# Performance work log

Hardware: AMD Instinct MI355X
Metric: run time of the kernel (lower is better)

## Reference

```python
import jax, jax.numpy as jnp
import numpy as np

N = 131072      # points (rays x samples chunk)
E = 8           # spatial sub-networks (centroids)
DIN = 90        # encoded pos+dir features fed to sub-NeRFs (xyz_real=True -> x[:, 3:])
H = 256         # sub-NeRF hidden width
DOUT = 4        # rgb + sigma
MARGIN = 2.0    # boundary_margin
EPS = 1e-8


def setup_inputs() -> dict:
    key = jax.random.key(0)
    k = jax.random.split(key, 5)
    x_xyz = jax.random.uniform(k[0], (N, 3), dtype=jnp.float32)          # routing coords in [0,1)^3
    x_feat = jax.random.normal(k[1], (N, DIN), dtype=jnp.float32)        # encoded features
    x = jnp.concatenate([x_xyz, x_feat], axis=1)                         # [N, 3+DIN]
    centroids = jax.random.uniform(k[2], (E, 3), dtype=jnp.float32)
    W1 = jax.random.normal(k[3], (E, DIN, H), dtype=jnp.float32) * 0.05
    b1 = jnp.zeros((E, H), dtype=jnp.float32)
    W2 = jax.random.normal(k[4], (E, H, DOUT), dtype=jnp.float32) * 0.05
    b2 = jnp.zeros((E, DOUT), dtype=jnp.float32)
    return {"x": x, "centroids": centroids, "W1": W1, "b1": b1, "W2": W2, "b2": b2}


def reference(x, centroids, W1, b1, W2, b2):
    # --- centroid routing (torch.cdist equivalent) ---
    xyz = x[:, :3]                                                       # [N,3]
    d2 = jnp.sum((xyz[:, None, :] - centroids[None, :, :]) ** 2, axis=-1)
    dist = jnp.sqrt(jnp.maximum(d2, 0.0))                                # [N,E]
    inv = 1.0 / (dist + EPS)
    min_d = jnp.min(dist, axis=1, keepdims=True)                         # [N,1]
    inv = jnp.where(dist > MARGIN * min_d, 0.0, inv)                     # zero far experts
    weights = inv / jnp.sum(inv, axis=-1, keepdims=True)                 # [N,E], rows sum to 1

    # --- per-expert sub-NeRF MLP, weighted combine ---
    # Dense-equivalent of masked gather + weighted scatter-add: experts whose
    # weight is exactly 0 contribute nothing, matching the torch masked path.
    feat = x[:, 3:]                                                      # xyz_real=True -> drop xyz
    h = jax.nn.relu(jnp.einsum('nd,edh->enh', feat, W1) + b1[:, None, :])  # [E,N,H]
    out_e = jnp.einsum('enh,eho->eno', h, W2) + b2[:, None, :]             # [E,N,DOUT]
    return jnp.einsum('eno,ne->no', out_e, weights)                        # [N,DOUT]
```

## Files before the change

kernel.cpp:

```cpp
#include <hip/hip_runtime.h>

#define NPTS 131072
#define NE 8
#define DIN 90
#define NH 256

typedef __attribute__((ext_vector_type(8))) short bf16x8;
typedef __attribute__((ext_vector_type(4))) float f32x4;
typedef __attribute__((ext_vector_type(2))) float f32x2;
typedef __attribute__((ext_vector_type(4))) unsigned int u32x4;
typedef __attribute__((ext_vector_type(2))) unsigned int u32x2;
typedef __attribute__((ext_vector_type(4), aligned(4))) float f32x4a;
typedef __attribute__((ext_vector_type(2), aligned(4))) float f32x2a;

__device__ __forceinline__ unsigned short f2bf(float f) {
  unsigned int u = __float_as_uint(f);
  u += 0x7fffu + ((u >> 16) & 1u);
  return (unsigned short)(u >> 16);
}

__device__ __forceinline__ unsigned int pkbf(float f0, float f1) {
  unsigned int u0 = __float_as_uint(f0) + 0x7fffu;
  unsigned int u1 = __float_as_uint(f1) + 0x7fffu;
  return __builtin_amdgcn_perm(u1, u0, 0x07060302u);
}

__device__ __forceinline__ bf16x8 cvt8(f32x4 a, f32x4 b) {
  u32x4 r;
  r[0] = pkbf(a[0], a[1]);
  r[1] = pkbf(a[2], a[3]);
  r[2] = pkbf(b[0], b[1]);
  r[3] = pkbf(b[2], b[3]);
  return __builtin_bit_cast(bf16x8, r);
}

#define PREP_T (184320 + 12288 + 8192 + 24576)
__global__ __launch_bounds__(256) void prep(const float* __restrict__ W1,
                                            const float* __restrict__ W2,
                                            unsigned short* __restrict__ W1T,
                                            unsigned short* __restrict__ W2T) {
  int tid = blockIdx.x * 256 + threadIdx.x;
  if (tid < 184320) {
    float v = W1[tid];
    int n = tid & 255, r = tid >> 8;
    int kp = r % 90, e = r / 90;
    W1T[(size_t)(e * NH + n) * 96 + kp] = f2bf(v);
    return;
  }
  tid -= 184320;
  if (tid < 12288) {
    int kp = 90 + tid % 6, q = tid / 6;
    int n = q & 255, e = q >> 8;
    W1T[(size_t)(e * NH + n) * 96 + kp] = 0;
    return;
  }
  tid -= 12288;
  if (tid < 8192) {
    float v = W2[tid];
    int o = tid & 3, k = (tid >> 2) & 255, e = tid >> 10;
    W2T[(size_t)(e * 16 + o) * NH + k] = f2bf(v);
    return;
  }
  tid -= 8192;
  if (tid < 24576) {
    int k = tid & 255, q = tid >> 8;
    int o = 4 + q % 12, e = q / 12;
    W2T[(size_t)(e * 16 + o) * NH + k] = 0;
  }
}

__global__ __launch_bounds__(256, 3) void meganerf_main(
    const float* __restrict__ x, const float* __restrict__ cent,
    const float* __restrict__ b1, const float* __restrict__ b2,
    const unsigned short* __restrict__ W1T, const unsigned short* __restrict__ W2T,
    float* __restrict__ out) {
  __shared__ unsigned short sH[4 * 4096];
  __shared__ float sW[NE][64];
  __shared__ float sB2[64][4];

  const int t    = threadIdx.x;
  const int lane = t & 63;
  const int wid  = t >> 6;
  const int l15  = lane & 15;
  const int l4   = lane >> 4;
  const int row0 = blockIdx.x * 64;
  const int gbase = wid * 4096;

  bf16x8 bfr[4][3];
#pragma unroll
  for (int nf = 0; nf < 4; ++nf) {
    const float* gr = x + (size_t)(row0 + 16 * nf + l15) * 93 + 3;
    f32x4 v0, v1;
    v0 = *(const f32x4a*)(gr + 8 * l4);
    v1 = *(const f32x4a*)(gr + 8 * l4 + 4);
    bfr[nf][0] = cvt8(v0, v1);
    v0 = *(const f32x4a*)(gr + 32 + 8 * l4);
    v1 = *(const f32x4a*)(gr + 36 + 8 * l4);
    bfr[nf][1] = cvt8(v0, v1);
    if (l4 < 3) {
      v0 = *(const f32x4a*)(gr + 64 + 8 * l4);
      v1 = *(const f32x4a*)(gr + 68 + 8 * l4);
    } else {
      f32x2 tl = *(const f32x2a*)(gr + 88);
      v0[0] = tl[0]; v0[1] = tl[1]; v0[2] = 0.f; v0[3] = 0.f;
      v1[0] = 0.f; v1[1] = 0.f; v1[2] = 0.f; v1[3] = 0.f;
    }
    bfr[nf][2] = cvt8(v0, v1);
  }

  if (t < 64) {
    const float* gx = x + (size_t)(row0 + t) * 93;
    float px = gx[0], py = gx[1], pz = gx[2];
    float dist[NE], inv[NE];
    float mind = 3.4e38f;
#pragma unroll
    for (int e = 0; e < NE; ++e) {
      float dx = px - cent[e * 3 + 0];
      float dy = py - cent[e * 3 + 1];
      float dz = pz - cent[e * 3 + 2];
      float d2 = dx * dx + dy * dy + dz * dz;
      float d = sqrtf(fmaxf(d2, 0.f));
      dist[e] = d;
      inv[e] = 1.f / (d + 1e-8f);
      mind = fminf(mind, d);
    }
    float s = 0.f;
#pragma unroll
    for (int e = 0; e < NE; ++e) {
      if (dist[e] > 2.0f * mind) inv[e] = 0.f;
      s += inv[e];
    }
    float rs = 1.f / s;
    float bb[4] = {0.f, 0.f, 0.f, 0.f};
#pragma unroll
    for (int e = 0; e < NE; ++e) {
      float w = inv[e] * rs;
      sW[e][t] = w;
#pragma unroll
      for (int o = 0; o < 4; ++o) bb[o] += w * b2[e * 4 + o];
    }
#pragma unroll
    for (int o = 0; o < 4; ++o) sB2[t][o] = bb[o];
  }
  __syncthreads();

  f32x4 facc[4] = {{0.f, 0.f, 0.f, 0.f}, {0.f, 0.f, 0.f, 0.f},
                   {0.f, 0.f, 0.f, 0.f}, {0.f, 0.f, 0.f, 0.f}};

  for (int e = 0; e < NE; ++e) {
    bf16x8 bw[2];
#pragma unroll
    for (int ks2 = 0; ks2 < 2; ++ks2)
      bw[ks2] = *(const bf16x8*)(W2T + (size_t)(e * 16 + l15) * NH +
                                 128 * ks2 + 32 * wid + 8 * l4);
    float wv[4];
#pragma unroll
    for (int nf = 0; nf < 4; ++nf) wv[nf] = sW[e][16 * nf + l15];

#pragma unroll
    for (int c = 0; c < 2; ++c) {
      const int colbase = 128 * c + 32 * wid;
      bf16x8 w1f[2][3];
#pragma unroll
      for (int ks = 0; ks < 3; ++ks)
#pragma unroll
        for (int mf = 0; mf < 2; ++mf)
          w1f[mf][ks] = *(const bf16x8*)(W1T +
              (size_t)(e * NH + colbase + 16 * mf + l15) * 96 + 32 * ks + 8 * l4);
      f32x4 b1v[2];
#pragma unroll
      for (int mf = 0; mf < 2; ++mf)
        b1v[mf] = *(const f32x4*)(b1 + e * NH + colbase + 16 * mf + 4 * l4);
      f32x4 acc[2][4];
#pragma unroll
      for (int mf = 0; mf < 2; ++mf)
#pragma unroll
        for (int nf = 0; nf < 4; ++nf) acc[mf][nf] = b1v[mf];
#pragma unroll
      for (int ks = 0; ks < 3; ++ks)
#pragma unroll
        for (int mf = 0; mf < 2; ++mf)
#pragma unroll
          for (int nf = 0; nf < 4; ++nf)
            acc[mf][nf] = __builtin_amdgcn_mfma_f32_16x16x32_bf16(
                w1f[mf][ks], bfr[nf][ks], acc[mf][nf], 0, 0, 0);

#pragma unroll
      for (int mf = 0; mf < 2; ++mf) {
#pragma unroll
        for (int nf = 0; nf < 4; ++nf) {
          const float w = wv[nf];
          f32x4 a = acc[mf][nf];
          f32x2 p0, p1;
          p0[0] = a[0]; p0[1] = a[1];
          p1[0] = a[2]; p1[1] = a[3];
          const f32x2 z = {0.f, 0.f};
          p0 = __builtin_elementwise_max(p0, z) * w;
          p1 = __builtin_elementwise_max(p1, z) * w;
          u32x2 pk;
          pk[0] = pkbf(p0[0], p0[1]);
          pk[1] = pkbf(p1[0], p1[1]);
          *(u32x2*)&sH[gbase + ((nf * 2 + c) * 64 + (l15 + 16 * (2 * mf + (l4 >> 1)))) * 8 +
                       4 * (l4 & 1)] = pk;
        }
      }
    }

#pragma unroll
    for (int ks2 = 0; ks2 < 2; ++ks2)
#pragma unroll
      for (int rf = 0; rf < 4; ++rf) {
        bf16x8 ah = *(const bf16x8*)&sH[gbase + ((rf * 2 + ks2) * 64 + lane) * 8];
        facc[rf] = __builtin_amdgcn_mfma_f32_16x16x32_bf16(ah, bw[ks2], facc[rf], 0, 0, 0);
      }
  }

  __syncthreads();
  float* sOutP = (float*)sH;
  if (l15 < 4) {
#pragma unroll
    for (int rf = 0; rf < 4; ++rf)
#pragma unroll
      for (int r = 0; r < 4; ++r)
        sOutP[(wid * 64 + 16 * rf + 4 * l4 + r) * 4 + l15] = facc[rf][r];
  }
  __syncthreads();
  {
    const int row = t >> 2, o = t & 3;
    float v = sB2[row][o] + sOutP[(0 * 64 + row) * 4 + o] + sOutP[(1 * 64 + row) * 4 + o] +
              sOutP[(2 * 64 + row) * 4 + o] + sOutP[(3 * 64 + row) * 4 + o];
    out[row0 * 4 + t] = v;
  }
}

extern "C" void kernel_launch(void* const* d_in, const int* in_sizes, int n_in,
                              void* d_out, int out_size, void* d_ws, size_t ws_size,
                              hipStream_t stream) {
  const float* x    = (const float*)d_in[0];
  const float* cent = (const float*)d_in[1];
  const float* W1   = (const float*)d_in[2];
  const float* b1   = (const float*)d_in[3];
  const float* W2   = (const float*)d_in[4];
  const float* b2   = (const float*)d_in[5];
  float* out = (float*)d_out;

  unsigned short* W1T = (unsigned short*)d_ws;
  unsigned short* W2T = W1T + NE * NH * 96;

  prep<<<(PREP_T + 255) / 256, 256, 0, stream>>>(W1, W2, W1T, W2T);
  meganerf_main<<<NPTS / 64, 256, 0, stream>>>(x, cent, b1, b2, W1T, W2T, out);
}
```

Baseline: 168.1 us.

## Double-buffer W1 fragments across flattened expert/chunk loop and stage b1 in LDS

Flattens the expert×column-chunk loop into 16 iterations and prefetches the next iteration's W1 fragments into a second register buffer while the current MFMAs run. The second-layer MFMAs are issued per chunk instead of once per expert. Bias b1 is copied to shared memory once per block, and bf16 packing uses the hardware cvt_pk_bf16_f32 instruction when the compiler provides it, which rounds properly instead of the add-0x7fff trick. The extra register buffer raises VGPR pressure and may hurt occupancy at the 3-blocks launch bound, and sB1 adds 8KB of LDS per block.

Measured after the change: 168.6 us. No clear change (+0.3%).

```diff
diff --git a/kernel.cpp b/kernel.cpp
--- a/kernel.cpp
+++ b/kernel.cpp
@@ -19,11 +19,19 @@
   return (unsigned short)(u >> 16);
 }
 
+#if defined(__has_builtin) && __has_builtin(__builtin_amdgcn_cvt_pk_bf16_f32)
+typedef __attribute__((ext_vector_type(2))) __bf16 bf16x2;
+__device__ __forceinline__ unsigned int pkbf(float f0, float f1) {
+  bf16x2 r = __builtin_amdgcn_cvt_pk_bf16_f32(f0, f1);
+  return __builtin_bit_cast(unsigned int, r);
+}
+#else
 __device__ __forceinline__ unsigned int pkbf(float f0, float f1) {
   unsigned int u0 = __float_as_uint(f0) + 0x7fffu;
   unsigned int u1 = __float_as_uint(f1) + 0x7fffu;
   return __builtin_amdgcn_perm(u1, u0, 0x07060302u);
 }
+#endif
 
 __device__ __forceinline__ bf16x8 cvt8(f32x4 a, f32x4 b) {
   u32x4 r;
@@ -77,6 +85,7 @@
   __shared__ unsigned short sH[4 * 4096];
   __shared__ float sW[NE][64];
   __shared__ float sB2[64][4];
+  __shared__ float sB1[NE * NH];
 
   const int t    = threadIdx.x;
   const int lane = t & 63;
@@ -85,6 +94,10 @@
   const int l4   = lane >> 4;
   const int row0 = blockIdx.x * 64;
   const int gbase = wid * 4096;
+
+#pragma unroll
+  for (int j = 0; j < 2; ++j)
+    *(f32x4*)&sB1[t * 4 + j * 1024] = *(const f32x4a*)&b1[t * 4 + j * 1024];
 
   bf16x8 bfr[4][3];
 #pragma unroll
@@ -144,75 +157,81 @@
   }
   __syncthreads();
 
+  bf16x8 w1buf[2][6];
+  float wv[4];
+
+  auto loadW1 = [&](int idx, int buf) {
+    const int e = idx >> 1, c = idx & 1;
+    const unsigned short* p =
+        W1T + (size_t)(e * NH + 128 * c + 32 * wid + l15) * 96 + 8 * l4;
+#pragma unroll
+    for (int mf = 0; mf < 2; ++mf)
+#pragma unroll
+      for (int ks = 0; ks < 3; ++ks)
+        w1buf[buf][mf * 3 + ks] = *(const bf16x8*)(p + mf * (16 * 96) + 32 * ks);
+  };
+
+  loadW1(0, 0);
+
   f32x4 facc[4] = {{0.f, 0.f, 0.f, 0.f}, {0.f, 0.f, 0.f, 0.f},
                    {0.f, 0.f, 0.f, 0.f}, {0.f, 0.f, 0.f, 0.f}};
 
-  for (int e = 0; e < NE; ++e) {
-    bf16x8 bw[2];
-#pragma unroll
-    for (int ks2 = 0; ks2 < 2; ++ks2)
-      bw[ks2] = *(const bf16x8*)(W2T + (size_t)(e * 16 + l15) * NH +
-                                 128 * ks2 + 32 * wid + 8 * l4);
-    float wv[4];
-#pragma unroll
-    for (int nf = 0; nf < 4; ++nf) wv[nf] = sW[e][16 * nf + l15];
-
-#pragma unroll
-    for (int c = 0; c < 2; ++c) {
-      const int colbase = 128 * c + 32 * wid;
-      bf16x8 w1f[2][3];
-#pragma unroll
-      for (int ks = 0; ks < 3; ++ks)
-#pragma unroll
-        for (int mf = 0; mf < 2; ++mf)
-          w1f[mf][ks] = *(const bf16x8*)(W1T +
-              (size_t)(e * NH + colbase + 16 * mf + l15) * 96 + 32 * ks + 8 * l4);
-      f32x4 b1v[2];
+#pragma unroll 2
+  for (int i = 0; i < 16; ++i) {
+    const int e = i >> 1, c = i & 1, cur = i & 1, nxt = cur ^ 1;
+    loadW1((i + 1) & 15, nxt);
+
+    const int colbase = 128 * c + 32 * wid;
+    bf16x8 bw = *(const bf16x8*)(W2T + (size_t)(e * 16 + l15) * NH + colbase + 8 * l4);
+    if (c == 0) {
+#pragma unroll
+      for (int nf = 0; nf < 4; ++nf) wv[nf] = sW[e][16 * nf + l15];
+    }
+    f32x4 b1v[2];
+#pragma unroll
+    for (int mf = 0; mf < 2; ++mf)
+      b1v[mf] = *(const f32x4*)&sB1[e * NH + colbase + 16 * mf + 4 * l4];
+
+    f32x4 acc[2][4];
+#pragma unroll
+    for (int mf = 0; mf < 2; ++mf)
+#pragma unroll
+      for (int nf = 0; nf < 4; ++nf)
+        acc[mf][nf] = __builtin_amdgcn_mfma_f32_16x16x32_bf16(
+            w1buf[cur][mf * 3 + 0], bfr[nf][0], b1v[mf], 0, 0, 0);
+#pragma unroll
+    for (int ks = 1; ks < 3; ++ks)
 #pragma unroll
       for (int mf = 0; mf < 2; ++mf)
-        b1v[mf] = *(const f32x4*)(b1 + e * NH + colbase + 16 * mf + 4 * l4);
-      f32x4 acc[2][4];
-#pragma unroll
-      for (int mf = 0; mf < 2; ++mf)
-#pragma unroll
-        for (int nf = 0; nf < 4; ++nf) acc[mf][nf] = b1v[mf];
-#pragma unroll
-      for (int ks = 0; ks < 3; ++ks)
-#pragma unroll
-        for (int mf = 0; mf < 2; ++mf)
-#pragma unroll
-          for (int nf = 0; nf < 4; ++nf)
-            acc[mf][nf] = __builtin_amdgcn_mfma_f32_16x16x32_bf16(
-                w1f[mf][ks], bfr[nf][ks], acc[mf][nf], 0, 0, 0);
-
-#pragma unroll
-      for (int mf = 0; mf < 2; ++mf) {
-#pragma unroll
-        for (int nf = 0; nf < 4; ++nf) {
-          const float w = wv[nf];
-          f32x4 a = acc[mf][nf];
-          f32x2 p0, p1;
-          p0[0] = a[0]; p0[1] = a[1];
-          p1[0] = a[2]; p1[1] = a[3];
-          const f32x2 z = {0.f, 0.f};
-          p0 = __builtin_elementwise_max(p0, z) * w;
-          p1 = __builtin_elementwise_max(p1, z) * w;
-          u32x2 pk;
-          pk[0] = pkbf(p0[0], p0[1]);
-          pk[1] = pkbf(p1[0], p1[1]);
-          *(u32x2*)&sH[gbase + ((nf * 2 + c) * 64 + (l15 + 16 * (2 * mf + (l4 >> 1)))) * 8 +
-                       4 * (l4 & 1)] = pk;
-        }
+#pragma unroll
+        for (int nf = 0; nf < 4; ++nf)
+          acc[mf][nf] = __builtin_amdgcn_mfma_f32_16x16x32_bf16(
+              w1buf[cur][mf * 3 + ks], bfr[nf][ks], acc[mf][nf], 0, 0, 0);
+
+#pragma unroll
+    for (int mf = 0; mf < 2; ++mf)
+#pragma unroll
+      for (int nf = 0; nf < 4; ++nf) {
+        const float w = wv[nf];
+        f32x4 a = acc[mf][nf];
+        f32x2 p0, p1;
+        p0[0] = a[0]; p0[1] = a[1];
+        p1[0] = a[2]; p1[1] = a[3];
+        const f32x2 z = {0.f, 0.f};
+        p0 = __builtin_elementwise_max(p0, z) * w;
+        p1 = __builtin_elementwise_max(p1, z) * w;
+        u32x2 pk;
+        pk[0] = pkbf(p0[0], p0[1]);
+        pk[1] = pkbf(p1[0], p1[1]);
+        *(u32x2*)&sH[gbase + ((nf * 2 + c) * 64 + (l15 + 16 * (2 * mf + (l4 >> 1)))) * 8 +
+                     4 * (l4 & 1)] = pk;
       }
-    }
-
-#pragma unroll
-    for (int ks2 = 0; ks2 < 2; ++ks2)
-#pragma unroll
-      for (int rf = 0; rf < 4; ++rf) {
-        bf16x8 ah = *(const bf16x8*)&sH[gbase + ((rf * 2 + ks2) * 64 + lane) * 8];
-        facc[rf] = __builtin_amdgcn_mfma_f32_16x16x32_bf16(ah, bw[ks2], facc[rf], 0, 0, 0);
-      }
+
+#pragma unroll
+    for (int rf = 0; rf < 4; ++rf) {
+      bf16x8 ah = *(const bf16x8*)&sH[gbase + ((rf * 2 + c) * 64 + lane) * 8];
+      facc[rf] = __builtin_amdgcn_mfma_f32_16x16x32_bf16(ah, bw, facc[rf], 0, 0, 0);
+    }
   }
 
   __syncthreads();
```
